# Kernel optimization log

Hardware: AMD Instinct MI355X
Metric: run time of the kernel (lower is better)

Reference implementation:

```python
import jax, jax.numpy as jnp
import numpy as np

N_NODES = 100000
N_EDGES = 640000
D_FEAT = 128


def setup_inputs() -> dict:
    key = jax.random.key(0)
    k1, k2, k3, k4 = jax.random.split(key, 4)
    input = jax.random.normal(k1, (N_NODES, D_FEAT), dtype=jnp.float32)
    eidx = jax.random.randint(k2, (2, N_EDGES), 0, N_NODES, dtype=jnp.int64)
    enorm = jax.random.uniform(k3, (N_EDGES,), dtype=jnp.float32)
    esgn = jnp.sign(jax.random.normal(k4, (N_EDGES,), dtype=jnp.float32))
    return {"input": input, "eidx": eidx, "enorm": enorm, "esgn": esgn}


def reference(input, eidx, enorm, esgn):
    # gather source features, scale by sign*norm, scatter-add into targets
    sidx, tidx = eidx[0], eidx[1]
    message = input[sidx] * (esgn * enorm)[:, None]  # [E, D]
    res = jax.ops.segment_sum(message, tidx, num_segments=input.shape[0])
    return res
```

## Files before the change

### kernel.cpp

```cpp
#include <hip/hip_runtime.h>
#include <hip/hip_bf16.h>

#define D_FEAT  128
#define CAP     16
#define OVFCAP  65536
#define CHUNK   512


__device__ __forceinline__ unsigned short f32_to_bf16_rne(float x) {
    union { float f; unsigned int u; } v; v.f = x;
    unsigned int r = v.u + 0x7fffu + ((v.u >> 16) & 1u);
    return (unsigned short)(r >> 16);
}

__global__ __launch_bounds__(256) void convfill_kernel(
    const float* __restrict__ in,
    const int* __restrict__ sidx, const int* __restrict__ tidx,
    const float* __restrict__ enorm, const float* __restrict__ esgn,
    unsigned short* __restrict__ bhalf,
    int* __restrict__ cnt,
    int2* __restrict__ bucket,
    int4* __restrict__ ovf,
    int convBlocks, int nConvThreads, int nE, int nN)
{
    if ((int)blockIdx.x < convBlocks) {
        int i = blockIdx.x * 256 + threadIdx.x;
        if (i >= nConvThreads) return;
        const float4* ip = reinterpret_cast<const float4*>(in) + (size_t)i * 2;
        float4 a = ip[0];
        float4 b = ip[1];
        union { int4 q; unsigned short u[8]; } o;
        o.u[0] = f32_to_bf16_rne(a.x); o.u[1] = f32_to_bf16_rne(a.y);
        o.u[2] = f32_to_bf16_rne(a.z); o.u[3] = f32_to_bf16_rne(a.w);
        o.u[4] = f32_to_bf16_rne(b.x); o.u[5] = f32_to_bf16_rne(b.y);
        o.u[6] = f32_to_bf16_rne(b.z); o.u[7] = f32_to_bf16_rne(b.w);
        reinterpret_cast<int4*>(bhalf)[i] = o.q;
    } else {
        int e = (blockIdx.x - convBlocks) * 256 + threadIdx.x;
        if (e >= nE) return;
        int t = tidx[e];
        int s = sidx[e];
        float w = esgn[e] * enorm[e];
        int pos = atomicAdd(&cnt[t], 1);
        if (pos < CAP) {
            bucket[(size_t)t * CAP + pos] = make_int2(s, __float_as_int(w));
        } else {
            int p = atomicAdd(&cnt[nN], 1);
            if (p < OVFCAP) ovf[p] = make_int4(s, t, __float_as_int(w), 0);
        }
    }
}

__global__ __launch_bounds__(256) void gather_bf16(
    const unsigned short* __restrict__ bhalf,
    const int*  __restrict__ cnt,
    const int2* __restrict__ bucket,
    const int4* __restrict__ ovf,
    float* __restrict__ out, int nN)
{
    long long gid = (long long)blockIdx.x * blockDim.x + threadIdx.x;
    int node = (int)(gid >> 4);
    int lane = (int)(gid & 15);
    if (node >= nN) return;

    int degRaw = cnt[node];
    int deg = degRaw > CAP ? CAP : degRaw;

    int2 myrec = bucket[(size_t)node * CAP + lane];
    int wl = threadIdx.x & 63;
    int gbase = wl & 48;

    float a0 = 0.f, a1 = 0.f, a2 = 0.f, a3 = 0.f;
    float a4 = 0.f, a5 = 0.f, a6 = 0.f, a7 = 0.f;

    #define ROW_ACC(Sv, Wv)                                                     \
    do {                                                                        \
        const int4* rp = reinterpret_cast<const int4*>(                         \
            bhalf + (size_t)(Sv) * D_FEAT);                                     \
        int4 q = rp[lane];                                                      \
        float w_ = (Wv);                                                        \
        unsigned int x0 = (unsigned int)q.x, x1 = (unsigned int)q.y;            \
        unsigned int x2 = (unsigned int)q.z, x3 = (unsigned int)q.w;            \
        a0 += __int_as_float((int)(x0 << 16)) * w_;                             \
        a1 += __int_as_float((int)(x0 & 0xffff0000u)) * w_;                     \
        a2 += __int_as_float((int)(x1 << 16)) * w_;                             \
        a3 += __int_as_float((int)(x1 & 0xffff0000u)) * w_;                     \
        a4 += __int_as_float((int)(x2 << 16)) * w_;                             \
        a5 += __int_as_float((int)(x2 & 0xffff0000u)) * w_;                     \
        a6 += __int_as_float((int)(x3 << 16)) * w_;                             \
        a7 += __int_as_float((int)(x3 & 0xffff0000u)) * w_;                     \
    } while (0)

    int j = 0;
    for (; j + 4 <= deg; j += 4) {
        int s0 = __shfl(myrec.x, gbase + j + 0, 64);
        int w0 = __shfl(myrec.y, gbase + j + 0, 64);
        int s1 = __shfl(myrec.x, gbase + j + 1, 64);
        int w1 = __shfl(myrec.y, gbase + j + 1, 64);
        int s2 = __shfl(myrec.x, gbase + j + 2, 64);
        int w2 = __shfl(myrec.y, gbase + j + 2, 64);
        int s3 = __shfl(myrec.x, gbase + j + 3, 64);
        int w3 = __shfl(myrec.y, gbase + j + 3, 64);
        ROW_ACC(s0, __int_as_float(w0));
        ROW_ACC(s1, __int_as_float(w1));
        ROW_ACC(s2, __int_as_float(w2));
        ROW_ACC(s3, __int_as_float(w3));
    }
    for (; j < deg; ++j) {
        int s0 = __shfl(myrec.x, gbase + j, 64);
        int w0 = __shfl(myrec.y, gbase + j, 64);
        ROW_ACC(s0, __int_as_float(w0));
    }

    if (degRaw > CAP) {
        int novf = cnt[nN];
        if (novf > OVFCAP) novf = OVFCAP;
        for (int k = 0; k < novf; ++k) {
            int4 r = ovf[k];
            if (r.y == node) ROW_ACC(r.x, __int_as_float(r.z));
        }
    }
    #undef ROW_ACC

    float* orow = out + (size_t)node * D_FEAT + (size_t)lane * 8;
    reinterpret_cast<float4*>(orow)[0] = make_float4(a0, a1, a2, a3);
    reinterpret_cast<float4*>(orow)[1] = make_float4(a4, a5, a6, a7);
}


__global__ __launch_bounds__(256) void fill_bucket(
    const int* __restrict__ sidx, const int* __restrict__ tidx,
    const float* __restrict__ enorm, const float* __restrict__ esgn,
    int* __restrict__ cnt, int2* __restrict__ bucket,
    int4* __restrict__ ovf, int nE, int nN)
{
    int e = blockIdx.x * blockDim.x + threadIdx.x;
    if (e >= nE) return;
    int t = tidx[e];
    int s = sidx[e];
    float w = esgn[e] * enorm[e];
    int pos = atomicAdd(&cnt[t], 1);
    if (pos < CAP) {
        bucket[(size_t)t * CAP + pos] = make_int2(s, __float_as_int(w));
    } else {
        int p = atomicAdd(&cnt[nN], 1);
        ovf[p] = make_int4(s, t, __float_as_int(w), 0);
    }
}

__global__ __launch_bounds__(256) void gather_bucket(
    const float* __restrict__ in, const int* __restrict__ cnt,
    const int2* __restrict__ bucket, float* __restrict__ out, int nNodes)
{
    long long gid = (long long)blockIdx.x * blockDim.x + threadIdx.x;
    int node = (int)(gid >> 4);
    int lane = (int)(gid & 15);
    if (node >= nNodes) return;

    int deg = cnt[node];
    if (deg > CAP) deg = CAP;
    const int2* eb = bucket + (size_t)node * CAP;

    float4 a0 = make_float4(0.f, 0.f, 0.f, 0.f);
    float4 a1 = make_float4(0.f, 0.f, 0.f, 0.f);
    int j = 0;
    for (; j + 2 <= deg; j += 2) {
        int2 e0 = eb[j];
        int2 e1 = eb[j + 1];
        const float4* r0 = reinterpret_cast<const float4*>(in + (size_t)e0.x * D_FEAT);
        const float4* r1 = reinterpret_cast<const float4*>(in + (size_t)e1.x * D_FEAT);
        float4 v00 = r0[lane];
        float4 v01 = r0[lane + 16];
        float4 v10 = r1[lane];
        float4 v11 = r1[lane + 16];
        float w0 = __int_as_float(e0.y);
        float w1 = __int_as_float(e1.y);
        a0.x += v00.x * w0; a0.y += v00.y * w0; a0.z += v00.z * w0; a0.w += v00.w * w0;
        a1.x += v01.x * w0; a1.y += v01.y * w0; a1.z += v01.z * w0; a1.w += v01.w * w0;
        a0.x += v10.x * w1; a0.y += v10.y * w1; a0.z += v10.z * w1; a0.w += v10.w * w1;
        a1.x += v11.x * w1; a1.y += v11.y * w1; a1.z += v11.z * w1; a1.w += v11.w * w1;
    }
    if (j < deg) {
        int2 e0 = eb[j];
        const float4* r0 = reinterpret_cast<const float4*>(in + (size_t)e0.x * D_FEAT);
        float4 v00 = r0[lane];
        float4 v01 = r0[lane + 16];
        float w0 = __int_as_float(e0.y);
        a0.x += v00.x * w0; a0.y += v00.y * w0; a0.z += v00.z * w0; a0.w += v00.w * w0;
        a1.x += v01.x * w0; a1.y += v01.y * w0; a1.z += v01.z * w0; a1.w += v01.w * w0;
    }
    float4* orow = reinterpret_cast<float4*>(out + (size_t)node * D_FEAT);
    orow[lane]      = a0;
    orow[lane + 16] = a1;
}

__global__ __launch_bounds__(256) void ovf_scatter(
    const float* __restrict__ in, const int* __restrict__ cnt,
    const int4* __restrict__ ovf, float* __restrict__ out, int nN)
{
    int novf = cnt[nN];
    long long total = (long long)novf * 32;
    long long stride = (long long)gridDim.x * blockDim.x;
    for (long long gid = (long long)blockIdx.x * blockDim.x + threadIdx.x;
         gid < total; gid += stride) {
        int e = (int)(gid >> 5);
        int lane = (int)(gid & 31);
        int4 r = ovf[e];
        float w = __int_as_float(r.z);
        float4 v = reinterpret_cast<const float4*>(in + (size_t)r.x * D_FEAT)[lane];
        float* dst = out + (size_t)r.y * D_FEAT + (size_t)lane * 4;
        atomicAdd(dst + 0, v.x * w);
        atomicAdd(dst + 1, v.y * w);
        atomicAdd(dst + 2, v.z * w);
        atomicAdd(dst + 3, v.w * w);
    }
}


__global__ __launch_bounds__(256) void hist_kernel(
    const int* __restrict__ tidx, int* __restrict__ cnt, int nE)
{
    int e = blockIdx.x * blockDim.x + threadIdx.x;
    if (e < nE) atomicAdd(&cnt[tidx[e]], 1);
}

__global__ __launch_bounds__(CHUNK) void scan_chunks(
    const int* __restrict__ cnt, int* __restrict__ offs,
    int* __restrict__ bsums, int n)
{
    __shared__ int sh[CHUNK];
    int i = blockIdx.x * CHUNK + threadIdx.x;
    int v = (i < n) ? cnt[i] : 0;
    sh[threadIdx.x] = v;
    __syncthreads();
    for (int d = 1; d < CHUNK; d <<= 1) {
        int t = sh[threadIdx.x];
        int u = (threadIdx.x >= d) ? sh[threadIdx.x - d] : 0;
        __syncthreads();
        sh[threadIdx.x] = t + u;
        __syncthreads();
    }
    int incl = sh[threadIdx.x];
    if (i < n) offs[i] = incl - v;
    if (threadIdx.x == CHUNK - 1) bsums[blockIdx.x] = incl;
}

__global__ __launch_bounds__(256) void scan_bsums(
    int* __restrict__ bsums, int nb)
{
    __shared__ int sh[256];
    int v = (threadIdx.x < nb) ? bsums[threadIdx.x] : 0;
    sh[threadIdx.x] = v;
    __syncthreads();
    for (int d = 1; d < 256; d <<= 1) {
        int t = sh[threadIdx.x];
        int u = (threadIdx.x >= d) ? sh[threadIdx.x - d] : 0;
        __syncthreads();
        sh[threadIdx.x] = t + u;
        __syncthreads();
    }
    if (threadIdx.x < nb) bsums[threadIdx.x] = sh[threadIdx.x] - v;
}

__global__ __launch_bounds__(256) void fill_csr(
    const int* __restrict__ sidx, const int* __restrict__ tidx,
    const float* __restrict__ enorm, const float* __restrict__ esgn,
    int* __restrict__ offs, const int* __restrict__ bsums,
    int2* __restrict__ edges, int nE)
{
    int e = blockIdx.x * blockDim.x + threadIdx.x;
    if (e >= nE) return;
    int t = tidx[e];
    int pos = bsums[t >> 9] + atomicAdd(&offs[t], 1);
    float w = esgn[e] * enorm[e];
    edges[pos] = make_int2(sidx[e], __float_as_int(w));
}

__global__ __launch_bounds__(256) void gather_kernel(
    const float* __restrict__ in, const int* __restrict__ offs,
    const int* __restrict__ bsums, const int2* __restrict__ edges,
    float* __restrict__ out, int nNodes)
{
    long long gid = (long long)blockIdx.x * blockDim.x + threadIdx.x;
    int node = (int)(gid >> 4);
    int lane = (int)(gid & 15);
    if (node >= nNodes) return;

    int base = bsums[node >> 9];
    int beg  = base + ((node & 511) ? offs[node - 1] : 0);
    int end  = base + offs[node];

    float4 a0 = make_float4(0.f, 0.f, 0.f, 0.f);
    float4 a1 = make_float4(0.f, 0.f, 0.f, 0.f);
    for (int j = beg; j < end; ++j) {
        int2 e0 = edges[j];
        const float4* r0 = reinterpret_cast<const float4*>(in + (size_t)e0.x * D_FEAT);
        float4 v00 = r0[lane];
        float4 v01 = r0[lane + 16];
        float w0 = __int_as_float(e0.y);
        a0.x += v00.x * w0; a0.y += v00.y * w0; a0.z += v00.z * w0; a0.w += v00.w * w0;
        a1.x += v01.x * w0; a1.y += v01.y * w0; a1.z += v01.z * w0; a1.w += v01.w * w0;
    }
    float4* orow = reinterpret_cast<float4*>(out + (size_t)node * D_FEAT);
    orow[lane]      = a0;
    orow[lane + 16] = a1;
}

__global__ __launch_bounds__(256) void graphconv_scatter(
    const float* __restrict__ in, const int* __restrict__ sidx,
    const int* __restrict__ tidx, const float* __restrict__ enorm,
    const float* __restrict__ esgn, float* __restrict__ out, int nE)
{
    long long gid = (long long)blockIdx.x * blockDim.x + threadIdx.x;
    int edge = (int)(gid >> 5);
    int lane = (int)(gid & 31);
    if (edge >= nE) return;
    int s = sidx[edge];
    int t = tidx[edge];
    float w = esgn[edge] * enorm[edge];
    float4 v = reinterpret_cast<const float4*>(in + (size_t)s * D_FEAT)[lane];
    float* dst = out + (size_t)t * D_FEAT + (size_t)lane * 4;
    atomicAdd(dst + 0, v.x * w);
    atomicAdd(dst + 1, v.y * w);
    atomicAdd(dst + 2, v.z * w);
    atomicAdd(dst + 3, v.w * w);
}

extern "C" void kernel_launch(void* const* d_in, const int* in_sizes, int n_in,
                              void* d_out, int out_size, void* d_ws, size_t ws_size,
                              hipStream_t stream) {
    const float* input = (const float*)d_in[0];
    const int*   eidx  = (const int*)d_in[1];
    const float* enorm = (const float*)d_in[2];
    const float* esgn  = (const float*)d_in[3];
    float* out = (float*)d_out;

    const int nE = in_sizes[2];
    const int nN = out_size / D_FEAT;
    const int* sidx = eidx;
    const int* tidx = eidx + nE;

    int eg = (nE + 255) / 256;

    size_t bhalf_bytes  = (size_t)nN * D_FEAT * 2;
    size_t bucketA_b    = (size_t)nN * CAP * 8;
    size_t ovfA_b       = (size_t)OVFCAP * 16;
    size_t cnt_bytes    = ((size_t)nN + 1) * 4;
    size_t need_A       = bhalf_bytes + bucketA_b + ovfA_b + cnt_bytes;

    size_t ovfB_b  = (size_t)nE * 16;
    size_t need_B  = bucketA_b + ovfB_b + cnt_bytes;

    const int nb = (nN + CHUNK - 1) / CHUNK;
    size_t need_C = ((size_t)nN + 256 + 2 * (size_t)nE) * 4;

    if (ws_size >= need_A) {
        unsigned short* bhalf = (unsigned short*)d_ws;
        int2* bucket = (int2*)((char*)d_ws + bhalf_bytes);
        int4* ovf    = (int4*)((char*)d_ws + bhalf_bytes + bucketA_b);
        int*  cnt    = (int*)((char*)d_ws + bhalf_bytes + bucketA_b + ovfA_b);

        hipMemsetAsync(cnt, 0, cnt_bytes, stream);

        int nConvThreads = nN * (D_FEAT / 8);
        int convBlocks = (nConvThreads + 255) / 256;
        int totBlocks = convBlocks + eg;
        convfill_kernel<<<totBlocks, 256, 0, stream>>>(
            input, sidx, tidx, enorm, esgn, bhalf, cnt, bucket, ovf,
            convBlocks, nConvThreads, nE, nN);

        long long gthreads = (long long)nN * 16;
        int ggrid = (int)((gthreads + 255) / 256);
        gather_bf16<<<ggrid, 256, 0, stream>>>(bhalf, cnt, bucket, ovf, out, nN);
    } else if (ws_size >= need_B) {
        int2* bucket = (int2*)d_ws;
        int4* ovf    = (int4*)((char*)d_ws + bucketA_b);
        int*  cnt    = (int*)((char*)d_ws + bucketA_b + ovfB_b);

        hipMemsetAsync(cnt, 0, cnt_bytes, stream);
        fill_bucket<<<eg, 256, 0, stream>>>(sidx, tidx, enorm, esgn,
                                            cnt, bucket, ovf, nE, nN);
        long long gthreads = (long long)nN * 16;
        int ggrid = (int)((gthreads + 255) / 256);
        gather_bucket<<<ggrid, 256, 0, stream>>>(input, cnt, bucket, out, nN);
        ovf_scatter<<<256, 256, 0, stream>>>(input, cnt, ovf, out, nN);
    } else if (ws_size >= need_C && nb <= 256) {
        int*  offs  = (int*)d_ws;
        int*  bsums = offs + nN;
        int2* edges = (int2*)(bsums + 256);

        hipMemsetAsync(offs, 0, (size_t)nN * 4, stream);
        hist_kernel<<<eg, 256, 0, stream>>>(tidx, offs, nE);
        scan_chunks<<<nb, CHUNK, 0, stream>>>(offs, offs, bsums, nN);
        scan_bsums<<<1, 256, 0, stream>>>(bsums, nb);
        fill_csr<<<eg, 256, 0, stream>>>(sidx, tidx, enorm, esgn,
                                         offs, bsums, edges, nE);
        long long gthreads = (long long)nN * 16;
        int ggrid = (int)((gthreads + 255) / 256);
        gather_kernel<<<ggrid, 256, 0, stream>>>(input, offs, bsums, edges,
                                                 out, nN);
    } else {
        hipMemsetAsync(d_out, 0, (size_t)out_size * 4, stream);
        long long tthreads = (long long)nE * 32;
        int grid = (int)((tthreads + 255) / 256);
        graphconv_scatter<<<grid, 256, 0, stream>>>(input, sidx, tidx, enorm,
                                                    esgn, out, nE);
    }
}
```

Before: 103.5 us.

## Interleave edge-bucketing blocks with conversion blocks and batch 8 edges per thread

The fused convert/fill kernel now spreads the edge-bucketing blocks evenly among the bf16 conversion blocks instead of placing them all after the conversion blocks. Each edge thread handles 8 edges, issuing all loads and then all atomics so several atomics are in flight at once. The goal is to overlap the latency-bound atomic work with the bandwidth-bound conversion and to keep more memory operations outstanding per thread. In exchange it adds block-index arithmetic, extra registers per edge thread, and uneven per-block work.

```diff
diff --git a/kernel.cpp b/kernel.cpp
--- a/kernel.cpp
+++ b/kernel.cpp
@@ -4,6 +4,7 @@
 #define D_FEAT  128
 #define CAP     16
 #define OVFCAP  65536
+#define EPT     8
 #define CHUNK   512
 
 
@@ -21,10 +22,45 @@
     int* __restrict__ cnt,
     int2* __restrict__ bucket,
     int4* __restrict__ ovf,
-    int convBlocks, int nConvThreads, int nE, int nN)
-{
-    if ((int)blockIdx.x < convBlocks) {
-        int i = blockIdx.x * 256 + threadIdx.x;
+    int R, int edgeBlocks, int nConvThreads, int nE, int nN)
+{
+    int bid = (int)blockIdx.x;
+    int er  = bid / R;
+    bool isEdge = ((bid % R) == 0) && (er < edgeBlocks);
+
+    if (isEdge) {
+        int base = er * (256 * EPT) + (int)threadIdx.x;
+        int t[EPT], s[EPT], p[EPT];
+        float w[EPT];
+        #pragma unroll
+        for (int k = 0; k < EPT; ++k) {
+            int e = base + k * 256;
+            if (e < nE) {
+                t[k] = tidx[e];
+                s[k] = sidx[e];
+                w[k] = esgn[e] * enorm[e];
+            } else {
+                t[k] = -1; s[k] = 0; w[k] = 0.f;
+            }
+        }
+        #pragma unroll
+        for (int k = 0; k < EPT; ++k)
+            p[k] = (t[k] >= 0) ? atomicAdd(&cnt[t[k]], 1) : 0;
+        #pragma unroll
+        for (int k = 0; k < EPT; ++k) {
+            if (t[k] < 0) continue;
+            if (p[k] < CAP) {
+                bucket[(size_t)t[k] * CAP + p[k]] =
+                    make_int2(s[k], __float_as_int(w[k]));
+            } else {
+                int q = atomicAdd(&cnt[nN], 1);
+                if (q < OVFCAP)
+                    ovf[q] = make_int4(s[k], t[k], __float_as_int(w[k]), 0);
+            }
+        }
+    } else {
+        int convIdx = bid - min(er + 1, edgeBlocks);
+        int i = convIdx * 256 + (int)threadIdx.x;
         if (i >= nConvThreads) return;
         const float4* ip = reinterpret_cast<const float4*>(in) + (size_t)i * 2;
         float4 a = ip[0];
@@ -35,19 +71,6 @@
         o.u[4] = f32_to_bf16_rne(b.x); o.u[5] = f32_to_bf16_rne(b.y);
         o.u[6] = f32_to_bf16_rne(b.z); o.u[7] = f32_to_bf16_rne(b.w);
         reinterpret_cast<int4*>(bhalf)[i] = o.q;
-    } else {
-        int e = (blockIdx.x - convBlocks) * 256 + threadIdx.x;
-        if (e >= nE) return;
-        int t = tidx[e];
-        int s = sidx[e];
-        float w = esgn[e] * enorm[e];
-        int pos = atomicAdd(&cnt[t], 1);
-        if (pos < CAP) {
-            bucket[(size_t)t * CAP + pos] = make_int2(s, __float_as_int(w));
-        } else {
-            int p = atomicAdd(&cnt[nN], 1);
-            if (p < OVFCAP) ovf[p] = make_int4(s, t, __float_as_int(w), 0);
-        }
     }
 }
 
@@ -364,10 +387,13 @@
 
         int nConvThreads = nN * (D_FEAT / 8);
         int convBlocks = (nConvThreads + 255) / 256;
-        int totBlocks = convBlocks + eg;
+        int edgeBlocks = (nE + 256 * EPT - 1) / (256 * EPT);
+        int totBlocks  = convBlocks + edgeBlocks;
+        int R = totBlocks / edgeBlocks;
+        if (R < 1) R = 1;
         convfill_kernel<<<totBlocks, 256, 0, stream>>>(
             input, sidx, tidx, enorm, esgn, bhalf, cnt, bucket, ovf,
-            convBlocks, nConvThreads, nE, nN);
+            R, edgeBlocks, nConvThreads, nE, nN);
 
         long long gthreads = (long long)nN * 16;
         int ggrid = (int)((gthreads + 255) / 256);
```

New measurement: 109.9 us. +6.2%, slower.

## Interleave edge-bucketing blocks with conversion blocks and pad per-node counters

Applied to the files above, without the earlier changes.

Edge-bucketing blocks are spread evenly among the bf16 conversion blocks so that atomic-heavy and bandwidth-heavy work run at the same time instead of back to back. Per-node counters are padded by a stride of 16, 4 or 1 ints, chosen by the available workspace, to reduce cache-line sharing among atomics. In exchange, the counter memset grows and the gather kernel's counter reads become strided and uncoalesced.

```diff
diff --git a/kernel.cpp b/kernel.cpp
--- a/kernel.cpp
+++ b/kernel.cpp
@@ -21,10 +21,29 @@
     int* __restrict__ cnt,
     int2* __restrict__ bucket,
     int4* __restrict__ ovf,
-    int convBlocks, int nConvThreads, int nE, int nN)
-{
-    if ((int)blockIdx.x < convBlocks) {
-        int i = blockIdx.x * 256 + threadIdx.x;
+    int R, int edgeBlocks, int cstride, int nConvThreads, int nE, int nN)
+{
+    int bid = (int)blockIdx.x;
+    int er  = bid / R;
+    bool isEdge = ((bid % R) == 0) && (er < edgeBlocks);
+
+    if (isEdge) {
+        int e = er * 256 + (int)threadIdx.x;
+        if (e >= nE) return;
+        int t = tidx[e];
+        int s = sidx[e];
+        float w = esgn[e] * enorm[e];
+        int pos = atomicAdd(&cnt[(size_t)t * cstride], 1);
+        if (pos < CAP) {
+            bucket[(size_t)t * CAP + pos] = make_int2(s, __float_as_int(w));
+        } else {
+            int q = atomicAdd(&cnt[(size_t)nN * cstride], 1);
+            if (q < OVFCAP)
+                ovf[q] = make_int4(s, t, __float_as_int(w), 0);
+        }
+    } else {
+        int convIdx = bid - min(er + 1, edgeBlocks);
+        int i = convIdx * 256 + (int)threadIdx.x;
         if (i >= nConvThreads) return;
         const float4* ip = reinterpret_cast<const float4*>(in) + (size_t)i * 2;
         float4 a = ip[0];
@@ -35,19 +54,6 @@
         o.u[4] = f32_to_bf16_rne(b.x); o.u[5] = f32_to_bf16_rne(b.y);
         o.u[6] = f32_to_bf16_rne(b.z); o.u[7] = f32_to_bf16_rne(b.w);
         reinterpret_cast<int4*>(bhalf)[i] = o.q;
-    } else {
-        int e = (blockIdx.x - convBlocks) * 256 + threadIdx.x;
-        if (e >= nE) return;
-        int t = tidx[e];
-        int s = sidx[e];
-        float w = esgn[e] * enorm[e];
-        int pos = atomicAdd(&cnt[t], 1);
-        if (pos < CAP) {
-            bucket[(size_t)t * CAP + pos] = make_int2(s, __float_as_int(w));
-        } else {
-            int p = atomicAdd(&cnt[nN], 1);
-            if (p < OVFCAP) ovf[p] = make_int4(s, t, __float_as_int(w), 0);
-        }
     }
 }
 
@@ -56,14 +62,14 @@
     const int*  __restrict__ cnt,
     const int2* __restrict__ bucket,
     const int4* __restrict__ ovf,
-    float* __restrict__ out, int nN)
+    float* __restrict__ out, int cstride, int nN)
 {
     long long gid = (long long)blockIdx.x * blockDim.x + threadIdx.x;
     int node = (int)(gid >> 4);
     int lane = (int)(gid & 15);
     if (node >= nN) return;
 
-    int degRaw = cnt[node];
+    int degRaw = cnt[(size_t)node * cstride];
     int deg = degRaw > CAP ? CAP : degRaw;
 
     int2 myrec = bucket[(size_t)node * CAP + lane];
@@ -113,7 +119,7 @@
     }
 
     if (degRaw > CAP) {
-        int novf = cnt[nN];
+        int novf = cnt[(size_t)nN * cstride];
         if (novf > OVFCAP) novf = OVFCAP;
         for (int k = 0; k < novf; ++k) {
             int4 r = ovf[k];
@@ -342,19 +348,25 @@
 
     int eg = (nE + 255) / 256;
 
-    size_t bhalf_bytes  = (size_t)nN * D_FEAT * 2;
-    size_t bucketA_b    = (size_t)nN * CAP * 8;
-    size_t ovfA_b       = (size_t)OVFCAP * 16;
-    size_t cnt_bytes    = ((size_t)nN + 1) * 4;
-    size_t need_A       = bhalf_bytes + bucketA_b + ovfA_b + cnt_bytes;
-
-    size_t ovfB_b  = (size_t)nE * 16;
-    size_t need_B  = bucketA_b + ovfB_b + cnt_bytes;
+    size_t bhalf_bytes = (size_t)nN * D_FEAT * 2;
+    size_t bucketA_b   = (size_t)nN * CAP * 8;
+    size_t ovfA_b      = (size_t)OVFCAP * 16;
+    int cstride = 0;
+    size_t cnt_bytes = 0, need_A = 0;
+    for (int cs : {16, 4, 1}) {
+        size_t cb = ((size_t)nN * cs + 1) * 4;
+        size_t na = bhalf_bytes + bucketA_b + ovfA_b + cb;
+        if (ws_size >= na) { cstride = cs; cnt_bytes = cb; need_A = na; break; }
+    }
+
+    size_t ovfB_b   = (size_t)nE * 16;
+    size_t cntB_b   = ((size_t)nN + 1) * 4;
+    size_t need_B   = bucketA_b + ovfB_b + cntB_b;
 
     const int nb = (nN + CHUNK - 1) / CHUNK;
     size_t need_C = ((size_t)nN + 256 + 2 * (size_t)nE) * 4;
 
-    if (ws_size >= need_A) {
+    if (cstride > 0) {
         unsigned short* bhalf = (unsigned short*)d_ws;
         int2* bucket = (int2*)((char*)d_ws + bhalf_bytes);
         int4* ovf    = (int4*)((char*)d_ws + bhalf_bytes + bucketA_b);
@@ -364,20 +376,24 @@
 
         int nConvThreads = nN * (D_FEAT / 8);
         int convBlocks = (nConvThreads + 255) / 256;
-        int totBlocks = convBlocks + eg;
+        int edgeBlocks = eg;
+        int totBlocks  = convBlocks + edgeBlocks;
+        int R = totBlocks / edgeBlocks;
+        if (R < 1) R = 1;
         convfill_kernel<<<totBlocks, 256, 0, stream>>>(
             input, sidx, tidx, enorm, esgn, bhalf, cnt, bucket, ovf,
-            convBlocks, nConvThreads, nE, nN);
+            R, edgeBlocks, cstride, nConvThreads, nE, nN);
 
         long long gthreads = (long long)nN * 16;
         int ggrid = (int)((gthreads + 255) / 256);
-        gather_bf16<<<ggrid, 256, 0, stream>>>(bhalf, cnt, bucket, ovf, out, nN);
+        gather_bf16<<<ggrid, 256, 0, stream>>>(bhalf, cnt, bucket, ovf, out,
+                                               cstride, nN);
     } else if (ws_size >= need_B) {
         int2* bucket = (int2*)d_ws;
         int4* ovf    = (int4*)((char*)d_ws + bucketA_b);
         int*  cnt    = (int*)((char*)d_ws + bucketA_b + ovfB_b);
 
-        hipMemsetAsync(cnt, 0, cnt_bytes, stream);
+        hipMemsetAsync(cnt, 0, cntB_b, stream);
         fill_bucket<<<eg, 256, 0, stream>>>(sidx, tidx, enorm, esgn,
                                             cnt, bucket, ovf, nE, nN);
         long long gthreads = (long long)nN * 16;
```

Measured after the change: 86.82 us. -16.1%, faster.
